# Performance work log

Hardware: AMD Instinct MI355X
Metric: run time of the kernel (lower is better)

## Reference

```python
import jax, jax.numpy as jnp
import numpy as np

S, B, D, H = 1024, 64, 1024, 1024


def setup_inputs() -> dict:
    key = jax.random.key(0)
    ks = jax.random.split(key, 18)
    stdv = 1.0 / np.sqrt(H)  # per reset_parameters
    inp = {"Xt": jax.random.normal(ks[0], (S, B, D), dtype=jnp.float32)}
    wnames = ["iiW", "hiW", "ifW", "hfW", "igW", "hgW", "ioW", "hoW"]
    bnames = ["iiB", "hiB", "ifB", "hfB", "igB", "hgB", "ioB", "hoB"]
    for i, n in enumerate(wnames):
        inp[n] = jax.random.uniform(ks[1 + i], (H, D if n[0] == "i" else H),
                                    minval=-stdv, maxval=stdv, dtype=jnp.float32)
    for i, n in enumerate(bnames):
        inp[n] = jax.random.uniform(ks[9 + i], (H,), minval=-stdv, maxval=stdv,
                                    dtype=jnp.float32)
    return inp


def reference(Xt, iiW, hiW, ifW, hfW, igW, hgW, ioW, hoW,
              iiB, hiB, ifB, hfB, igB, hgB, ioB, hoB):
    # single-layer LSTM, batch_first=False: scan over seq dim 0.
    # Math matches torch forward_one: separate input/hidden linears per gate,
    # actF = actC = tanh, dropout = 0.
    bias_i = iiB + hiB  # fuse constant bias sums once
    bias_f = ifB + hfB
    bias_g = igB + hgB
    bias_o = ioB + hoB

    def step(carry, x):
        h, c = carry  # [B, H] each
        I = jax.nn.sigmoid(x @ iiW.T + h @ hiW.T + bias_i)
        F = jax.nn.sigmoid(x @ ifW.T + h @ hfW.T + bias_f)
        G = jnp.tanh(x @ igW.T + h @ hgW.T + bias_g)
        O = jax.nn.sigmoid(x @ ioW.T + h @ hoW.T + bias_o)
        c_ = F * c + I * G
        y = O * jnp.tanh(c_)
        return (y, c_), y

    h0 = jnp.zeros((Xt.shape[1], hiW.shape[0]), dtype=Xt.dtype)
    c0 = jnp.zeros_like(h0)
    (hT, cT), Yt = jax.lax.scan(step, (h0, c0), Xt)
    return Yt, hT, cT  # stack_output=True -> Yt is [S, B, H]
```

## Files before the change

### kernel.cpp

```cpp
#include <hip/hip_runtime.h>
#include <hip/hip_bf16.h>
#include <stdint.h>


#define NWG 128

typedef __attribute__((ext_vector_type(8))) short bf16x8;
typedef __attribute__((ext_vector_type(4))) float f32x4;

__device__ __forceinline__ unsigned short f2bf(float f) {
    unsigned u = __builtin_bit_cast(unsigned, f);
    return (unsigned short)((u + 0x7fffu + ((u >> 16) & 1u)) >> 16);
}

__global__ void init_kernel(const float* __restrict__ iiB, const float* __restrict__ hiB,
                            const float* __restrict__ ifB, const float* __restrict__ hfB,
                            const float* __restrict__ igB, const float* __restrict__ hgB,
                            const float* __restrict__ ioB, const float* __restrict__ hoB,
                            float* __restrict__ bias, unsigned short* __restrict__ hbuf0,
                            float* __restrict__ c_ws, unsigned int* __restrict__ bar) {
    int tid = blockIdx.x * 256 + threadIdx.x;
    if (tid < 64) bar[tid] = 0u;
    if (tid < 4096) {
        int g = tid >> 10, j = tid & 1023;
        const float* ib = (g == 0 ? iiB : g == 1 ? ifB : g == 2 ? igB : ioB);
        const float* hb = (g == 0 ? hiB : g == 1 ? hfB : g == 2 ? hgB : hoB);
        bias[tid] = ib[j] + hb[j];
    }
    for (int i = tid; i < 65536; i += 16384) {
        __hip_atomic_store(hbuf0 + i, (unsigned short)0, __ATOMIC_RELAXED, __HIP_MEMORY_SCOPE_AGENT);
        c_ws[i] = 0.f;
    }
}

__global__ void prep_weights(const float* __restrict__ iiW, const float* __restrict__ hiW,
                             const float* __restrict__ ifW, const float* __restrict__ hfW,
                             const float* __restrict__ igW, const float* __restrict__ hgW,
                             const float* __restrict__ ioW, const float* __restrict__ hoW,
                             unsigned short* __restrict__ Wx, unsigned short* __restrict__ Wh) {
    int n = blockIdx.x;
    int g = n >> 10, j = n & 1023;
    const float* wx = (g == 0 ? iiW : g == 1 ? ifW : g == 2 ? igW : ioW) + (size_t)j * 1024;
    const float* wh = (g == 0 ? hiW : g == 1 ? hfW : g == 2 ? hgW : hoW) + (size_t)j * 1024;
    int k = threadIdx.x * 4;
    float4 a = *(const float4*)(wx + k);
    float4 b = *(const float4*)(wh + k);
    ushort4 ra = { f2bf(a.x), f2bf(a.y), f2bf(a.z), f2bf(a.w) };
    ushort4 rb = { f2bf(b.x), f2bf(b.y), f2bf(b.z), f2bf(b.w) };
    *(ushort4*)(Wx + (size_t)n * 1024 + k) = ra;
    *(ushort4*)(Wh + (size_t)n * 1024 + k) = rb;
}

__global__ __launch_bounds__(256, 2) void xproj_gemm(const float* __restrict__ A,
                                                     const unsigned short* __restrict__ Wx,
                                                     const float* __restrict__ bias,
                                                     float* __restrict__ C) {
    __shared__ __align__(16) unsigned short Asm[128 * 32];
    __shared__ __align__(16) unsigned short Bsm[128 * 32];
    int tid = threadIdx.x;
    int lane = tid & 63, wv = tid >> 6;
    int l15 = lane & 15, l4 = lane >> 4;
    int wrow = wv >> 1, wcol = wv & 1;
    int bn0 = blockIdx.x * 128, bm0 = blockIdx.y * 128;
    f32x4 acc[4][4] = {};

    for (int kk = 0; kk < 32; ++kk) {
        int k0 = kk * 32;
        __syncthreads();
#pragma unroll
        for (int it = 0; it < 2; ++it) {
            int tau = it * 256 + tid;
            int row = tau >> 2, slot = tau & 3;
            const float* src = A + (size_t)(bm0 + row) * 1024 + k0 + slot * 8;
            float4 x0 = *(const float4*)src;
            float4 x1 = *(const float4*)(src + 4);
            bf16x8 pk;
            pk[0] = (short)f2bf(x0.x); pk[1] = (short)f2bf(x0.y);
            pk[2] = (short)f2bf(x0.z); pk[3] = (short)f2bf(x0.w);
            pk[4] = (short)f2bf(x1.x); pk[5] = (short)f2bf(x1.y);
            pk[6] = (short)f2bf(x1.z); pk[7] = (short)f2bf(x1.w);
            int dslot = slot ^ (row & 3);
            *(bf16x8*)((char*)Asm + row * 64 + dslot * 16) = pk;
        }
#pragma unroll
        for (int it = 0; it < 2; ++it) {
            int tau = it * 256 + tid;
            int row = tau >> 2, slot = tau & 3;
            int sslot = slot ^ (row & 3);
            const unsigned short* src = Wx + (size_t)(bn0 + row) * 1024 + k0 + sslot * 8;
            char* ldsb = (char*)Bsm + it * 4096 + wv * 1024;
            __builtin_amdgcn_global_load_lds((const __attribute__((address_space(1))) void*)src,
                                             (__attribute__((address_space(3))) void*)ldsb, 16, 0, 0);
        }
        __syncthreads();
        bf16x8 af[4], bfv[4];
#pragma unroll
        for (int i = 0; i < 4; ++i) {
            int rowa = wrow * 64 + i * 16 + l15;
            int sa = l4 ^ (rowa & 3);
            af[i] = *(const bf16x8*)((const char*)Asm + rowa * 64 + sa * 16);
            int rowb = wcol * 64 + i * 16 + l15;
            int sb = l4 ^ (rowb & 3);
            bfv[i] = *(const bf16x8*)((const char*)Bsm + rowb * 64 + sb * 16);
        }
#pragma unroll
        for (int i = 0; i < 4; ++i)
#pragma unroll
            for (int j = 0; j < 4; ++j)
                acc[i][j] = __builtin_amdgcn_mfma_f32_16x16x32_bf16(af[i], bfv[j], acc[i][j], 0, 0, 0);
    }
#pragma unroll
    for (int i = 0; i < 4; ++i) {
        int m = bm0 + wrow * 64 + i * 16 + l4 * 4;
#pragma unroll
        for (int j = 0; j < 4; ++j) {
            int n = bn0 + wcol * 64 + j * 16 + l15;
            float bs = bias[n];
#pragma unroll
            for (int r = 0; r < 4; ++r)
                C[(size_t)(m + r) * 4096 + n] = acc[i][j][r] + bs;
        }
    }
}

__global__ __launch_bounds__(256, 1) void lstm_steps(const float* __restrict__ xproj,
                                                     unsigned short* __restrict__ hbuf,
                                                     float* __restrict__ c_ws,
                                                     const unsigned short* __restrict__ Wh,
                                                     unsigned int* __restrict__ bar,
                                                     float* __restrict__ out,
                                                     int t0, int T) {
    __shared__ float red[8192];
    int tid = threadIdx.x, lane = tid & 63, wv = tid >> 6;
    int l15 = lane & 15, l4 = lane >> 4;
    int wg = blockIdx.x;
    int mhalf = wg & 1;
    int cg = wg >> 1;
    int j0 = cg * 16;
    unsigned int* mybar = bar + mhalf * 32;

    bf16x8 w[8][4];
#pragma unroll
    for (int ks = 0; ks < 8; ++ks)
#pragma unroll
        for (int g = 0; g < 4; ++g) {
            int n = g * 1024 + j0 + l15;
            int k = wv * 256 + ks * 32 + l4 * 8;
            w[ks][g] = *(const bf16x8*)(Wh + (size_t)n * 1024 + k);
        }

    float c_reg[2];
#pragma unroll
    for (int pi = 0; pi < 2; ++pi) {
        int p = wv * 2 + pi, m = p >> 2, r = p & 3;
        int b = mhalf * 32 + m * 16 + l4 * 4 + r;
        c_reg[pi] = c_ws[(size_t)b * 1024 + j0 + l15];
    }

    for (int tl = 0; tl < T; ++tl) {
        int ts = t0 + tl;
        int par = ts & 1;
        const unsigned short* hb = hbuf + (size_t)par * 65536;

        float xp[2][4];
#pragma unroll
        for (int pi = 0; pi < 2; ++pi) {
            int p = wv * 2 + pi, m = p >> 2, r = p & 3;
            int b = mhalf * 32 + m * 16 + l4 * 4 + r;
#pragma unroll
            for (int g = 0; g < 4; ++g)
                xp[pi][g] = xproj[(size_t)(tl * 64 + b) * 4096 + g * 1024 + j0 + l15];
        }

        bf16x8 af[2][8];
#pragma unroll
        for (int m = 0; m < 2; ++m) {
            int row = mhalf * 32 + m * 16 + l15;
            const unsigned short* rp = hb + (size_t)row * 1024 + wv * 256 + l4 * 8;
#pragma unroll
            for (int ks = 0; ks < 8; ++ks) {
                unsigned long long* p = (unsigned long long*)(rp + ks * 32);
                union { unsigned long long q[2]; bf16x8 v; } u;
                u.q[0] = __hip_atomic_load(p,     __ATOMIC_RELAXED, __HIP_MEMORY_SCOPE_AGENT);
                u.q[1] = __hip_atomic_load(p + 1, __ATOMIC_RELAXED, __HIP_MEMORY_SCOPE_AGENT);
                af[m][ks] = u.v;
            }
        }

        f32x4 acc[2][4] = {};
#pragma unroll
        for (int ks = 0; ks < 8; ++ks)
#pragma unroll
            for (int m = 0; m < 2; ++m)
#pragma unroll
                for (int g = 0; g < 4; ++g)
                    acc[m][g] = __builtin_amdgcn_mfma_f32_16x16x32_bf16(af[m][ks], w[ks][g], acc[m][g], 0, 0, 0);

#pragma unroll
        for (int m = 0; m < 2; ++m)
#pragma unroll
            for (int g = 0; g < 4; ++g)
#pragma unroll
                for (int r = 0; r < 4; ++r)
                    red[(wv * 32 + m * 16 + g * 4 + r) * 64 + lane] = acc[m][g][r];
        __syncthreads();

        float yv[2];
#pragma unroll
        for (int pi = 0; pi < 2; ++pi) {
            int p = wv * 2 + pi, m = p >> 2, r = p & 3;
            int b = mhalf * 32 + m * 16 + l4 * 4 + r;
            int j = j0 + l15;
            float pre[4];
#pragma unroll
            for (int g = 0; g < 4; ++g) {
                int s = m * 16 + g * 4 + r;
                pre[g] = red[s * 64 + lane] + red[(32 + s) * 64 + lane] +
                         red[(64 + s) * 64 + lane] + red[(96 + s) * 64 + lane] + xp[pi][g];
            }
            float I = 1.f / (1.f + __expf(-pre[0]));
            float F = 1.f / (1.f + __expf(-pre[1]));
            float G = tanhf(pre[2]);
            float O = 1.f / (1.f + __expf(-pre[3]));
            float c = F * c_reg[pi] + I * G;
            c_reg[pi] = c;
            float y = O * tanhf(c);
            yv[pi] = y;
            __hip_atomic_store(hbuf + (size_t)(par ^ 1) * 65536 + (size_t)b * 1024 + j,
                               f2bf(y), __ATOMIC_RELAXED, __HIP_MEMORY_SCOPE_AGENT);
        }

        __syncthreads();
        if (tid == 0) {
            __hip_atomic_fetch_add(mybar, 1u, __ATOMIC_RELAXED, __HIP_MEMORY_SCOPE_AGENT);
            unsigned target = (unsigned)(ts + 1) * 64u;
            while (__hip_atomic_load(mybar, __ATOMIC_RELAXED, __HIP_MEMORY_SCOPE_AGENT) < target)
                __builtin_amdgcn_s_sleep(1);
        }
        __syncthreads();

#pragma unroll
        for (int pi = 0; pi < 2; ++pi) {
            int p = wv * 2 + pi, m = p >> 2, r = p & 3;
            int b = mhalf * 32 + m * 16 + l4 * 4 + r;
            int j = j0 + l15;
            out[(size_t)(ts * 64 + b) * 1024 + j] = yv[pi];
            if (ts == 1023) {
                out[67108864u + (size_t)b * 1024 + j] = yv[pi];
                out[67108864u + 65536u + (size_t)b * 1024 + j] = c_reg[pi];
            }
        }
    }
#pragma unroll
    for (int pi = 0; pi < 2; ++pi) {
        int p = wv * 2 + pi, m = p >> 2, r = p & 3;
        int b = mhalf * 32 + m * 16 + l4 * 4 + r;
        c_ws[(size_t)b * 1024 + j0 + l15] = c_reg[pi];
    }
}

extern "C" void kernel_launch(void* const* d_in, const int* in_sizes, int n_in,
                              void* d_out, int out_size, void* d_ws, size_t ws_size,
                              hipStream_t stream) {
    (void)in_sizes; (void)n_in; (void)out_size;
    const float* Xt = (const float*)d_in[0];
    const float* W[8]; for (int i = 0; i < 8; ++i) W[i] = (const float*)d_in[1 + i];
    const float* Bv[8]; for (int i = 0; i < 8; ++i) Bv[i] = (const float*)d_in[9 + i];
    float* out = (float*)d_out;
    uint8_t* ws = (uint8_t*)d_ws;

    unsigned int*  bar   = (unsigned int*)(ws + 0);
    float*         bias  = (float*)(ws + 256);
    unsigned short* hbuf = (unsigned short*)(ws + 16640);
    float*         c_ws  = (float*)(ws + 278784);
    unsigned short* Wx   = (unsigned short*)(ws + 540928);
    unsigned short* Wh   = (unsigned short*)(ws + 8929536);
    float*         xproj = (float*)(ws + 17318144);

    size_t avail = ws_size > 17318144 ? ws_size - 17318144 : 0;
    int T = 4;
    for (int t = 1024; t >= 4; t >>= 1)
        if ((size_t)t * 1048576ull <= avail) { T = t; break; }

    init_kernel<<<64, 256, 0, stream>>>(Bv[0], Bv[1], Bv[2], Bv[3], Bv[4], Bv[5], Bv[6], Bv[7],
                                        bias, hbuf, c_ws, bar);
    prep_weights<<<4096, 256, 0, stream>>>(W[0], W[1], W[2], W[3], W[4], W[5], W[6], W[7], Wx, Wh);

    int nch = 1024 / T;
    for (int c = 0; c < nch; ++c) {
        xproj_gemm<<<dim3(32, T / 2), 256, 0, stream>>>(Xt + (size_t)c * T * 65536, Wx, bias, xproj);
        lstm_steps<<<NWG, 256, 0, stream>>>(xproj, hbuf, c_ws, Wh, bar, out, c * T, T);
    }
}
```

Before: 7.792 ms.

## Halve workgroup count with 512-thread blocks, leader-based barrier, fast activations

The recurrent kernel now runs 64 workgroups of 512 threads, each covering two 16-column slices, which halves the number of blocks taking part in the per-step grid barrier. The barrier becomes arrive/release: one leader per batch half polls the arrival counter and publishes a release flag that the other blocks poll, cutting contention on the shared counter. Sigmoid and tanh use exp plus hardware reciprocal approximations instead of division and tanhf. In exchange each block holds twice the LDS, barrier latency now includes an extra leader hop, and the activations lose some accuracy.

New measurement: 10.97 ms. 1.41x slower.

```diff
diff --git a/kernel.cpp b/kernel.cpp
--- a/kernel.cpp
+++ b/kernel.cpp
@@ -3,14 +3,20 @@
 #include <stdint.h>
 
 
-#define NWG 128
-
 typedef __attribute__((ext_vector_type(8))) short bf16x8;
 typedef __attribute__((ext_vector_type(4))) float f32x4;
 
 __device__ __forceinline__ unsigned short f2bf(float f) {
     unsigned u = __builtin_bit_cast(unsigned, f);
     return (unsigned short)((u + 0x7fffu + ((u >> 16) & 1u)) >> 16);
+}
+__device__ __forceinline__ float fast_sigmoid(float x) {
+    return __builtin_amdgcn_rcpf(1.f + __expf(-x));
+}
+__device__ __forceinline__ float fast_tanh(float x) {
+    float xc = fminf(fmaxf(x, -9.f), 9.f);
+    float e = __expf(2.f * xc);
+    return (e - 1.f) * __builtin_amdgcn_rcpf(e + 1.f);
 }
 
 __global__ void init_kernel(const float* __restrict__ iiB, const float* __restrict__ hiB,
@@ -20,7 +26,7 @@
                             float* __restrict__ bias, unsigned short* __restrict__ hbuf0,
                             float* __restrict__ c_ws, unsigned int* __restrict__ bar) {
     int tid = blockIdx.x * 256 + threadIdx.x;
-    if (tid < 64) bar[tid] = 0u;
+    if (tid < 128) bar[tid] = 0u;
     if (tid < 4096) {
         int g = tid >> 10, j = tid & 1023;
         const float* ib = (g == 0 ? iiB : g == 1 ? ifB : g == 2 ? igB : ioB);
@@ -123,21 +129,24 @@
     }
 }
 
-__global__ __launch_bounds__(256, 1) void lstm_steps(const float* __restrict__ xproj,
+__global__ __launch_bounds__(512, 1) void lstm_steps(const float* __restrict__ xproj,
                                                      unsigned short* __restrict__ hbuf,
                                                      float* __restrict__ c_ws,
                                                      const unsigned short* __restrict__ Wh,
                                                      unsigned int* __restrict__ bar,
                                                      float* __restrict__ out,
                                                      int t0, int T) {
-    __shared__ float red[8192];
+    __shared__ float red[16384];
     int tid = threadIdx.x, lane = tid & 63, wv = tid >> 6;
     int l15 = lane & 15, l4 = lane >> 4;
     int wg = blockIdx.x;
     int mhalf = wg & 1;
-    int cg = wg >> 1;
-    int j0 = cg * 16;
-    unsigned int* mybar = bar + mhalf * 32;
+    int cgrp = wg >> 1;
+    int sg = wv >> 2, kw = wv & 3;
+    int j0 = cgrp * 32 + sg * 16;
+    unsigned int* arrive  = bar + mhalf * 32;
+    unsigned int* release = bar + 64 + mhalf * 32;
+    bool leader = (cgrp == 0);
 
     bf16x8 w[8][4];
 #pragma unroll
@@ -145,14 +154,14 @@
 #pragma unroll
         for (int g = 0; g < 4; ++g) {
             int n = g * 1024 + j0 + l15;
-            int k = wv * 256 + ks * 32 + l4 * 8;
+            int k = kw * 256 + ks * 32 + l4 * 8;
             w[ks][g] = *(const bf16x8*)(Wh + (size_t)n * 1024 + k);
         }
 
     float c_reg[2];
 #pragma unroll
     for (int pi = 0; pi < 2; ++pi) {
-        int p = wv * 2 + pi, m = p >> 2, r = p & 3;
+        int p = kw * 2 + pi, m = p >> 2, r = p & 3;
         int b = mhalf * 32 + m * 16 + l4 * 4 + r;
         c_reg[pi] = c_ws[(size_t)b * 1024 + j0 + l15];
     }
@@ -165,7 +174,7 @@
         float xp[2][4];
 #pragma unroll
         for (int pi = 0; pi < 2; ++pi) {
-            int p = wv * 2 + pi, m = p >> 2, r = p & 3;
+            int p = kw * 2 + pi, m = p >> 2, r = p & 3;
             int b = mhalf * 32 + m * 16 + l4 * 4 + r;
 #pragma unroll
             for (int g = 0; g < 4; ++g)
@@ -176,7 +185,7 @@
 #pragma unroll
         for (int m = 0; m < 2; ++m) {
             int row = mhalf * 32 + m * 16 + l15;
-            const unsigned short* rp = hb + (size_t)row * 1024 + wv * 256 + l4 * 8;
+            const unsigned short* rp = hb + (size_t)row * 1024 + kw * 256 + l4 * 8;
 #pragma unroll
             for (int ks = 0; ks < 8; ++ks) {
                 unsigned long long* p = (unsigned long long*)(rp + ks * 32);
@@ -208,23 +217,25 @@
         float yv[2];
 #pragma unroll
         for (int pi = 0; pi < 2; ++pi) {
-            int p = wv * 2 + pi, m = p >> 2, r = p & 3;
+            int p = kw * 2 + pi, m = p >> 2, r = p & 3;
             int b = mhalf * 32 + m * 16 + l4 * 4 + r;
             int j = j0 + l15;
             float pre[4];
 #pragma unroll
             for (int g = 0; g < 4; ++g) {
-                int s = m * 16 + g * 4 + r;
-                pre[g] = red[s * 64 + lane] + red[(32 + s) * 64 + lane] +
-                         red[(64 + s) * 64 + lane] + red[(96 + s) * 64 + lane] + xp[pi][g];
+                int ss = m * 16 + g * 4 + r;
+                pre[g] = red[((sg * 4 + 0) * 32 + ss) * 64 + lane] +
+                         red[((sg * 4 + 1) * 32 + ss) * 64 + lane] +
+                         red[((sg * 4 + 2) * 32 + ss) * 64 + lane] +
+                         red[((sg * 4 + 3) * 32 + ss) * 64 + lane] + xp[pi][g];
             }
-            float I = 1.f / (1.f + __expf(-pre[0]));
-            float F = 1.f / (1.f + __expf(-pre[1]));
-            float G = tanhf(pre[2]);
-            float O = 1.f / (1.f + __expf(-pre[3]));
+            float I = fast_sigmoid(pre[0]);
+            float F = fast_sigmoid(pre[1]);
+            float G = fast_tanh(pre[2]);
+            float O = fast_sigmoid(pre[3]);
             float c = F * c_reg[pi] + I * G;
             c_reg[pi] = c;
-            float y = O * tanhf(c);
+            float y = O * fast_tanh(c);
             yv[pi] = y;
             __hip_atomic_store(hbuf + (size_t)(par ^ 1) * 65536 + (size_t)b * 1024 + j,
                                f2bf(y), __ATOMIC_RELAXED, __HIP_MEMORY_SCOPE_AGENT);
@@ -232,16 +243,22 @@
 
         __syncthreads();
         if (tid == 0) {
-            __hip_atomic_fetch_add(mybar, 1u, __ATOMIC_RELAXED, __HIP_MEMORY_SCOPE_AGENT);
-            unsigned target = (unsigned)(ts + 1) * 64u;
-            while (__hip_atomic_load(mybar, __ATOMIC_RELAXED, __HIP_MEMORY_SCOPE_AGENT) < target)
-                __builtin_amdgcn_s_sleep(1);
+            __hip_atomic_fetch_add(arrive, 1u, __ATOMIC_RELAXED, __HIP_MEMORY_SCOPE_AGENT);
+            unsigned target = (unsigned)(ts + 1);
+            if (leader) {
+                while (__hip_atomic_load(arrive, __ATOMIC_RELAXED, __HIP_MEMORY_SCOPE_AGENT) < target * 32u)
+                    __builtin_amdgcn_s_sleep(1);
+                __hip_atomic_store(release, target, __ATOMIC_RELAXED, __HIP_MEMORY_SCOPE_AGENT);
+            } else {
+                while (__hip_atomic_load(release, __ATOMIC_RELAXED, __HIP_MEMORY_SCOPE_AGENT) < target)
+                    __builtin_amdgcn_s_sleep(1);
+            }
         }
         __syncthreads();
 
 #pragma unroll
         for (int pi = 0; pi < 2; ++pi) {
-            int p = wv * 2 + pi, m = p >> 2, r = p & 3;
+            int p = kw * 2 + pi, m = p >> 2, r = p & 3;
             int b = mhalf * 32 + m * 16 + l4 * 4 + r;
             int j = j0 + l15;
             out[(size_t)(ts * 64 + b) * 1024 + j] = yv[pi];
@@ -253,7 +270,7 @@
     }
 #pragma unroll
     for (int pi = 0; pi < 2; ++pi) {
-        int p = wv * 2 + pi, m = p >> 2, r = p & 3;
+        int p = kw * 2 + pi, m = p >> 2, r = p & 3;
         int b = mhalf * 32 + m * 16 + l4 * 4 + r;
         c_ws[(size_t)b * 1024 + j0 + l15] = c_reg[pi];
     }
@@ -270,14 +287,14 @@
     uint8_t* ws = (uint8_t*)d_ws;
 
     unsigned int*  bar   = (unsigned int*)(ws + 0);
-    float*         bias  = (float*)(ws + 256);
-    unsigned short* hbuf = (unsigned short*)(ws + 16640);
-    float*         c_ws  = (float*)(ws + 278784);
-    unsigned short* Wx   = (unsigned short*)(ws + 540928);
-    unsigned short* Wh   = (unsigned short*)(ws + 8929536);
-    float*         xproj = (float*)(ws + 17318144);
-
-    size_t avail = ws_size > 17318144 ? ws_size - 17318144 : 0;
+    float*         bias  = (float*)(ws + 512);
+    unsigned short* hbuf = (unsigned short*)(ws + 16896);
+    float*         c_ws  = (float*)(ws + 279040);
+    unsigned short* Wx   = (unsigned short*)(ws + 541184);
+    unsigned short* Wh   = (unsigned short*)(ws + 8929792);
+    float*         xproj = (float*)(ws + 17318400);
+
+    size_t avail = ws_size > 17318400 ? ws_size - 17318400 : 0;
     int T = 4;
     for (int t = 1024; t >= 4; t >>= 1)
         if ((size_t)t * 1048576ull <= avail) { T = t; break; }
@@ -289,6 +306,6 @@
     int nch = 1024 / T;
     for (int c = 0; c < nch; ++c) {
         xproj_gemm<<<dim3(32, T / 2), 256, 0, stream>>>(Xt + (size_t)c * T * 65536, Wx, bias, xproj);
-        lstm_steps<<<NWG, 256, 0, stream>>>(xproj, hbuf, c_ws, Wh, bar, out, c * T, T);
-    }
-}
+        lstm_steps<<<64, 512, 0, stream>>>(xproj, hbuf, c_ws, Wh, bar, out, c * T, T);
+    }
+}
```

## Interleave gate columns in xproj, prefetch next step's inputs, use fast activations

Applied to the files above, without the earlier changes.

The xproj GEMM now writes its output with the four gate values for each hidden unit interleaved, so the recurrent kernel fetches them with a single float4 load instead of four scattered loads. The next timestep's xproj values are loaded before the grid barrier spin, so that latency overlaps the wait. Sigmoid and tanh switch to exp plus hardware reciprocal approximations, with tanh clamped at ±9. The fast activations slightly change numerics, and the workspace offsets are shifted to make room for a larger barrier area.

After: 7.210 ms. 7.5% less time.

```diff
diff --git a/kernel.cpp b/kernel.cpp
--- a/kernel.cpp
+++ b/kernel.cpp
@@ -3,14 +3,20 @@
 #include <stdint.h>
 
 
-#define NWG 128
-
 typedef __attribute__((ext_vector_type(8))) short bf16x8;
 typedef __attribute__((ext_vector_type(4))) float f32x4;
 
 __device__ __forceinline__ unsigned short f2bf(float f) {
     unsigned u = __builtin_bit_cast(unsigned, f);
     return (unsigned short)((u + 0x7fffu + ((u >> 16) & 1u)) >> 16);
+}
+__device__ __forceinline__ float fast_sigmoid(float x) {
+    return __builtin_amdgcn_rcpf(1.f + __expf(-x));
+}
+__device__ __forceinline__ float fast_tanh(float x) {
+    float xc = fminf(fmaxf(x, -9.f), 9.f);
+    float e = __expf(2.f * xc);
+    return (e - 1.f) * __builtin_amdgcn_rcpf(e + 1.f);
 }
 
 __global__ void init_kernel(const float* __restrict__ iiB, const float* __restrict__ hiB,
@@ -20,7 +26,7 @@
                             float* __restrict__ bias, unsigned short* __restrict__ hbuf0,
                             float* __restrict__ c_ws, unsigned int* __restrict__ bar) {
     int tid = blockIdx.x * 256 + threadIdx.x;
-    if (tid < 64) bar[tid] = 0u;
+    if (tid < 128) bar[tid] = 0u;
     if (tid < 4096) {
         int g = tid >> 10, j = tid & 1023;
         const float* ib = (g == 0 ? iiB : g == 1 ? ifB : g == 2 ? igB : ioB);
@@ -115,10 +121,11 @@
 #pragma unroll
         for (int j = 0; j < 4; ++j) {
             int n = bn0 + wcol * 64 + j * 16 + l15;
+            int col = (n & 1023) * 4 + (n >> 10);
             float bs = bias[n];
 #pragma unroll
             for (int r = 0; r < 4; ++r)
-                C[(size_t)(m + r) * 4096 + n] = acc[i][j][r] + bs;
+                C[(size_t)(m + r) * 4096 + col] = acc[i][j][r] + bs;
         }
     }
 }
@@ -150,27 +157,23 @@
         }
 
     float c_reg[2];
+    int bq[2];
 #pragma unroll
     for (int pi = 0; pi < 2; ++pi) {
         int p = wv * 2 + pi, m = p >> 2, r = p & 3;
-        int b = mhalf * 32 + m * 16 + l4 * 4 + r;
-        c_reg[pi] = c_ws[(size_t)b * 1024 + j0 + l15];
-    }
+        bq[pi] = mhalf * 32 + m * 16 + l4 * 4 + r;
+        c_reg[pi] = c_ws[(size_t)bq[pi] * 1024 + j0 + l15];
+    }
+
+    float4 xp_cur[2];
+#pragma unroll
+    for (int pi = 0; pi < 2; ++pi)
+        xp_cur[pi] = *(const float4*)(xproj + (size_t)bq[pi] * 4096 + (j0 + l15) * 4);
 
     for (int tl = 0; tl < T; ++tl) {
         int ts = t0 + tl;
         int par = ts & 1;
         const unsigned short* hb = hbuf + (size_t)par * 65536;
-
-        float xp[2][4];
-#pragma unroll
-        for (int pi = 0; pi < 2; ++pi) {
-            int p = wv * 2 + pi, m = p >> 2, r = p & 3;
-            int b = mhalf * 32 + m * 16 + l4 * 4 + r;
-#pragma unroll
-            for (int g = 0; g < 4; ++g)
-                xp[pi][g] = xproj[(size_t)(tl * 64 + b) * 4096 + g * 1024 + j0 + l15];
-        }
 
         bf16x8 af[2][8];
 #pragma unroll
@@ -209,28 +212,36 @@
 #pragma unroll
         for (int pi = 0; pi < 2; ++pi) {
             int p = wv * 2 + pi, m = p >> 2, r = p & 3;
-            int b = mhalf * 32 + m * 16 + l4 * 4 + r;
+            int b = bq[pi];
             int j = j0 + l15;
+            const float* xpf = (const float*)&xp_cur[pi];
             float pre[4];
 #pragma unroll
             for (int g = 0; g < 4; ++g) {
                 int s = m * 16 + g * 4 + r;
                 pre[g] = red[s * 64 + lane] + red[(32 + s) * 64 + lane] +
-                         red[(64 + s) * 64 + lane] + red[(96 + s) * 64 + lane] + xp[pi][g];
+                         red[(64 + s) * 64 + lane] + red[(96 + s) * 64 + lane] + xpf[g];
             }
-            float I = 1.f / (1.f + __expf(-pre[0]));
-            float F = 1.f / (1.f + __expf(-pre[1]));
-            float G = tanhf(pre[2]);
-            float O = 1.f / (1.f + __expf(-pre[3]));
+            float I = fast_sigmoid(pre[0]);
+            float F = fast_sigmoid(pre[1]);
+            float G = fast_tanh(pre[2]);
+            float O = fast_sigmoid(pre[3]);
             float c = F * c_reg[pi] + I * G;
             c_reg[pi] = c;
-            float y = O * tanhf(c);
+            float y = O * fast_tanh(c);
             yv[pi] = y;
             __hip_atomic_store(hbuf + (size_t)(par ^ 1) * 65536 + (size_t)b * 1024 + j,
                                f2bf(y), __ATOMIC_RELAXED, __HIP_MEMORY_SCOPE_AGENT);
         }
 
         __syncthreads();
+
+        int tln = (tl + 1 < T) ? tl + 1 : tl;
+        float4 xp_nxt[2];
+#pragma unroll
+        for (int pi = 0; pi < 2; ++pi)
+            xp_nxt[pi] = *(const float4*)(xproj + (size_t)(tln * 64 + bq[pi]) * 4096 + (j0 + l15) * 4);
+
         if (tid == 0) {
             __hip_atomic_fetch_add(mybar, 1u, __ATOMIC_RELAXED, __HIP_MEMORY_SCOPE_AGENT);
             unsigned target = (unsigned)(ts + 1) * 64u;
@@ -241,8 +252,7 @@
 
 #pragma unroll
         for (int pi = 0; pi < 2; ++pi) {
-            int p = wv * 2 + pi, m = p >> 2, r = p & 3;
-            int b = mhalf * 32 + m * 16 + l4 * 4 + r;
+            int b = bq[pi];
             int j = j0 + l15;
             out[(size_t)(ts * 64 + b) * 1024 + j] = yv[pi];
             if (ts == 1023) {
@@ -250,13 +260,12 @@
                 out[67108864u + 65536u + (size_t)b * 1024 + j] = c_reg[pi];
             }
         }
-    }
-#pragma unroll
-    for (int pi = 0; pi < 2; ++pi) {
-        int p = wv * 2 + pi, m = p >> 2, r = p & 3;
-        int b = mhalf * 32 + m * 16 + l4 * 4 + r;
-        c_ws[(size_t)b * 1024 + j0 + l15] = c_reg[pi];
-    }
+        xp_cur[0] = xp_nxt[0];
+        xp_cur[1] = xp_nxt[1];
+    }
+#pragma unroll
+    for (int pi = 0; pi < 2; ++pi)
+        c_ws[(size_t)bq[pi] * 1024 + j0 + l15] = c_reg[pi];
 }
 
 extern "C" void kernel_launch(void* const* d_in, const int* in_sizes, int n_in,
@@ -270,14 +279,14 @@
     uint8_t* ws = (uint8_t*)d_ws;
 
     unsigned int*  bar   = (unsigned int*)(ws + 0);
-    float*         bias  = (float*)(ws + 256);
-    unsigned short* hbuf = (unsigned short*)(ws + 16640);
-    float*         c_ws  = (float*)(ws + 278784);
-    unsigned short* Wx   = (unsigned short*)(ws + 540928);
-    unsigned short* Wh   = (unsigned short*)(ws + 8929536);
-    float*         xproj = (float*)(ws + 17318144);
-
-    size_t avail = ws_size > 17318144 ? ws_size - 17318144 : 0;
+    float*         bias  = (float*)(ws + 512);
+    unsigned short* hbuf = (unsigned short*)(ws + 16896);
+    float*         c_ws  = (float*)(ws + 279040);
+    unsigned short* Wx   = (unsigned short*)(ws + 541184);
+    unsigned short* Wh   = (unsigned short*)(ws + 8929792);
+    float*         xproj = (float*)(ws + 17318400);
+
+    size_t avail = ws_size > 17318400 ? ws_size - 17318400 : 0;
     int T = 4;
     for (int t = 1024; t >= 4; t >>= 1)
         if ((size_t)t * 1048576ull <= avail) { T = t; break; }
@@ -289,6 +298,6 @@
     int nch = 1024 / T;
     for (int c = 0; c < nch; ++c) {
         xproj_gemm<<<dim3(32, T / 2), 256, 0, stream>>>(Xt + (size_t)c * T * 65536, Wx, bias, xproj);
-        lstm_steps<<<NWG, 256, 0, stream>>>(xproj, hbuf, c_ws, Wh, bar, out, c * T, T);
-    }
-}
+        lstm_steps<<<128, 256, 0, stream>>>(xproj, hbuf, c_ws, Wh, bar, out, c * T, T);
+    }
+}
```
